# Kernel optimization log

Measured on AMD Instinct MI355X. Metric: run time of the kernel, lower is better.

The kernel has to match this reference:

```python
import jax, jax.numpy as jnp
import numpy as np

H = 64        # hidden_channels (= per-head out_channels, concat=False)
HEADS = 4
N_SRC = 50000
N_TGT = 10000
E = 250000    # edges per direction
N_LBL = 200000


def setup_inputs() -> dict:
    key = jax.random.key(0)
    ks = jax.random.split(key, 16)
    s = 1.0 / np.sqrt(H)
    # stacked TransformerConv params: leading dims [layer=2, edge_type=2]
    # edge_type 0: source->target, edge_type 1: target->source
    Wq = jax.random.normal(ks[0], (2, 2, H, HEADS * H), jnp.float32) * s
    bq = jax.random.normal(ks[1], (2, 2, HEADS * H), jnp.float32) * 0.01
    Wk = jax.random.normal(ks[2], (2, 2, H, HEADS * H), jnp.float32) * s
    bk = jax.random.normal(ks[3], (2, 2, HEADS * H), jnp.float32) * 0.01
    Wv = jax.random.normal(ks[4], (2, 2, H, HEADS * H), jnp.float32) * s
    bv = jax.random.normal(ks[5], (2, 2, HEADS * H), jnp.float32) * 0.01
    Ws = jax.random.normal(ks[6], (2, 2, H, H), jnp.float32) * s  # skip (root) lin
    bs = jax.random.normal(ks[7], (2, 2, H), jnp.float32) * 0.01
    src_emb = jax.random.normal(ks[8], (N_SRC, H), jnp.float32)
    tgt_emb = jax.random.normal(ks[9], (N_TGT, H), jnp.float32)
    node_id_source = jnp.arange(N_SRC, dtype=jnp.int32)
    node_id_target = jnp.arange(N_TGT, dtype=jnp.int32)
    edge_index_st = jnp.stack([
        jax.random.randint(ks[10], (E,), 0, N_SRC),
        jax.random.randint(ks[11], (E,), 0, N_TGT)])
    edge_index_ts = jnp.stack([
        jax.random.randint(ks[12], (E,), 0, N_TGT),
        jax.random.randint(ks[13], (E,), 0, N_SRC)])
    edge_label_index = jnp.stack([
        jax.random.randint(ks[14], (N_LBL,), 0, N_SRC),
        jax.random.randint(ks[15], (N_LBL,), 0, N_TGT)])
    return {"src_emb": src_emb, "tgt_emb": tgt_emb,
            "Wq": Wq, "bq": bq, "Wk": Wk, "bk": bk, "Wv": Wv, "bv": bv,
            "Ws": Ws, "bs": bs,
            "node_id_source": node_id_source, "node_id_target": node_id_target,
            "edge_index_st": edge_index_st, "edge_index_ts": edge_index_ts,
            "edge_label_index": edge_label_index}


def _tconv(x_src, x_dst, edge, Wq, bq, Wk, bk, Wv, bv, Ws, bs):
    """PyG TransformerConv, heads=HEADS, concat=False (mean over heads), root_weight."""
    n_dst = x_dst.shape[0]
    q = (x_dst @ Wq + bq).reshape(n_dst, HEADS, H)            # [Ndst,h,d]
    k = (x_src @ Wk + bk).reshape(x_src.shape[0], HEADS, H)   # [Nsrc,h,d]
    v = (x_src @ Wv + bv).reshape(x_src.shape[0], HEADS, H)
    src, dst = edge[0], edge[1]
    # per-edge attention scores [E,h]
    score = jnp.einsum('ehd,ehd->eh', q[dst], k[src]) / jnp.sqrt(jnp.asarray(H, x_dst.dtype))
    m = jax.ops.segment_max(score, dst, num_segments=n_dst)   # segment softmax over in-edges
    e = jnp.exp(score - m[dst])
    denom = jax.ops.segment_sum(e, dst, num_segments=n_dst)[dst]
    alpha = e / denom
    out = jax.ops.segment_sum(alpha[..., None] * v[src], dst, num_segments=n_dst)  # [Ndst,h,d]
    return out.mean(axis=1) + x_dst @ Ws + bs


def reference(src_emb, tgt_emb, Wq, bq, Wk, bk, Wv, bv, Ws, bs,
              node_id_source, node_id_target, edge_index_st, edge_index_ts,
              edge_label_index):
    xs = src_emb[node_id_source]
    xt = tgt_emb[node_id_target]
    for l in range(2):
        xt_new = _tconv(xs, xt, edge_index_st, Wq[l, 0], bq[l, 0], Wk[l, 0], bk[l, 0],
                        Wv[l, 0], bv[l, 0], Ws[l, 0], bs[l, 0])
        xs_new = _tconv(xt, xs, edge_index_ts, Wq[l, 1], bq[l, 1], Wk[l, 1], bk[l, 1],
                        Wv[l, 1], bv[l, 1], Ws[l, 1], bs[l, 1])
        if l == 0:
            xs, xt = jax.nn.relu(xs_new), jax.nn.relu(xt_new)
        else:
            xs, xt = xs_new, xt_new
    # dot-product classifier over labeled (source, target) pairs
    pred = (xs[edge_label_index[0]] * xt[edge_label_index[1]]).sum(axis=-1)  # [N_LBL]
    return pred
```

## Files before the change

### kernel.cpp

```cpp
#include <hip/hip_runtime.h>

constexpr int NSRC = 50000;
constexpr int NTGT = 10000;
constexpr int NEDGE = 250000;
constexpr int NLBL = 200000;
constexpr int HD = 64;
constexpr int NH = 4;
constexpr int QK = 256;
constexpr int NTOT = NSRC + NTGT;

typedef __attribute__((ext_vector_type(8))) short bf16x8;
typedef __attribute__((ext_vector_type(4))) float f32x4;
typedef __attribute__((ext_vector_type(2))) float f32x2;

__device__ __forceinline__ unsigned short f2bf(float f) {
  unsigned u = __float_as_uint(f);
  u += 0x7FFFu + ((u >> 16) & 1u);
  return (unsigned short)(u >> 16);
}
__device__ __forceinline__ float bf2f(unsigned short b) {
  return __uint_as_float((unsigned)b << 16);
}
struct bf4 { unsigned short x, y, z, w; };
__device__ __forceinline__ float4 bf4_to_f4(bf4 u) {
  return make_float4(bf2f(u.x), bf2f(u.y), bf2f(u.z), bf2f(u.w));
}

template<int CTRL>
__device__ __forceinline__ float dpp_addf(float x) {
  int p = __builtin_amdgcn_update_dpp(0, __float_as_int(x), CTRL, 0xf, 0xf, true);
  return x + __int_as_float(p);
}
__device__ __forceinline__ float red16(float x) {
  x = dpp_addf<0xB1>(x);
  x = dpp_addf<0x4E>(x);
  x = dpp_addf<0x141>(x);
  x = dpp_addf<0x140>(x);
  return x;
}

__device__ __forceinline__ float dot4f(float4 q, float a, float b, float c, float d) {
  return fmaf(q.w, d, fmaf(q.z, c, fmaf(q.y, b, q.x * a)));
}

__global__ __launch_bounds__(256) void setup_kernel(
    const float* __restrict__ Wq, const float* __restrict__ Wk, const float* __restrict__ Wv,
    unsigned short* __restrict__ Wtq, unsigned short* __restrict__ Wtk, unsigned short* __restrict__ Wtv,
    const float* __restrict__ semb, const int* __restrict__ sids,
    const float* __restrict__ temb, const int* __restrict__ tids,
    float* __restrict__ xs, unsigned short* __restrict__ xsb,
    float* __restrict__ xt, unsigned short* __restrict__ xtb,
    int* __restrict__ counts, int nGatherBlk) {
  __shared__ float tile[64][65];
  int b = blockIdx.x;
  int t = threadIdx.x;
  if (b < 48) {
    int mat = b >> 2, ct = b & 3;
    int grp = mat >> 2, p = mat & 3;
    const float* W = (grp == 0) ? Wq : (grp == 1) ? Wk : Wv;
    unsigned short* Wt = (grp == 0) ? Wtq : (grp == 1) ? Wtk : Wtv;
    W += (size_t)p * 16384;
    Wt += (size_t)p * 16384;
    int c = t & 63, r4 = t >> 6;
    for (int rr = 0; rr < 64; rr += 4)
      tile[rr + r4][c] = W[(size_t)(rr + r4) * 256 + ct * 64 + c];
    __syncthreads();
    for (int rr = 0; rr < 64; rr += 4) {
      int nloc = rr + r4;
      Wt[(size_t)(ct * 64 + nloc) * 64 + c] = f2bf(tile[c][nloc]);
    }
  } else if (b < 48 + nGatherBlk) {
    int i = (b - 48) * 256 + t;
    if (i < NSRC * HD) {
      float v = semb[(size_t)sids[i >> 6] * HD + (i & 63)];
      xs[i] = v;
      xsb[i] = f2bf(v);
    } else if (i < NTOT * HD) {
      int j = i - NSRC * HD;
      float v = temb[(size_t)tids[j >> 6] * HD + (j & 63)];
      xt[j] = v;
      xtb[j] = f2bf(v);
    }
  } else {
    int i = (b - 48 - nGatherBlk) * 256 + t;
    if (i < NTOT) counts[i] = 0;
  }
}


__global__ __launch_bounds__(256) void hist_all_kernel(const int* __restrict__ e_st, const int* __restrict__ e_ts,
                                                       int* __restrict__ counts) {
  int i = blockIdx.x * 256 + threadIdx.x;
  if (i < NEDGE) atomicAdd(&counts[e_st[NEDGE + i]], 1);
  else if (i < 2 * NEDGE) atomicAdd(&counts[NTGT + e_ts[NEDGE + (i - NEDGE)]], 1);
}

__global__ __launch_bounds__(256) void scan1_kernel(const int* __restrict__ counts, int* __restrict__ incl,
                                                    int* __restrict__ blocksums, int n) {
  __shared__ int wtot[4];
  int t = threadIdx.x;
  int i0 = blockIdx.x * 1024 + t * 4;
  int e0 = (i0 + 0 < n) ? counts[i0 + 0] : 0;
  int e1 = (i0 + 1 < n) ? counts[i0 + 1] : 0;
  int e2 = (i0 + 2 < n) ? counts[i0 + 2] : 0;
  int e3 = (i0 + 3 < n) ? counts[i0 + 3] : 0;
  int s0 = e0, s1 = s0 + e1, s2 = s1 + e2, s3 = s2 + e3;
  int tsum = s3;
  int inc = tsum;
#pragma unroll
  for (int o = 1; o < 64; o <<= 1) {
    int u = __shfl_up(inc, o, 64);
    if ((t & 63) >= o) inc += u;
  }
  int wave = t >> 6;
  if ((t & 63) == 63) wtot[wave] = inc;
  __syncthreads();
  int woff = 0;
#pragma unroll
  for (int w_ = 0; w_ < 4; ++w_) if (w_ < wave) woff += wtot[w_];
  int toff = woff + inc - tsum;
  if (i0 + 0 < n) incl[i0 + 0] = toff + s0;
  if (i0 + 1 < n) incl[i0 + 1] = toff + s1;
  if (i0 + 2 < n) incl[i0 + 2] = toff + s2;
  if (i0 + 3 < n) incl[i0 + 3] = toff + s3;
  if (t == 255) blocksums[blockIdx.x] = woff + inc;
}

__global__ __launch_bounds__(64) void scan2_kernel(const int* __restrict__ blocksums, int* __restrict__ boff, int nb) {
  int t = threadIdx.x;
  int v = (t < nb) ? blocksums[t] : 0;
  int inc = v;
#pragma unroll
  for (int o = 1; o < 64; o <<= 1) {
    int u = __shfl_up(inc, o, 64);
    if (t >= o) inc += u;
  }
  if (t < nb) boff[t] = inc - v;
}

__global__ __launch_bounds__(256) void scan3_kernel(const int* __restrict__ incl, const int* __restrict__ counts,
                                                    const int* __restrict__ boff, int* __restrict__ rp_st,
                                                    int* __restrict__ rp_ts, int* __restrict__ cursor) {
  int i = blockIdx.x * 256 + threadIdx.x;
  if (i < NTOT) {
    int val = incl[i] + boff[i >> 10];
    if (i < NTGT) {
      rp_st[i + 1] = val;
      cursor[i] = val - counts[i];
      if (i == 0) rp_st[0] = 0;
    } else {
      int v2 = val - NEDGE;
      rp_ts[i - NTGT + 1] = v2;
      cursor[i] = v2 - counts[i];
      if (i == NTGT) rp_ts[0] = 0;
    }
  }
}

__global__ __launch_bounds__(256) void scatter_all_kernel(const int* __restrict__ e_st, const int* __restrict__ e_ts,
                                                          int* __restrict__ cursor, int* __restrict__ es_st,
                                                          int* __restrict__ es_ts) {
  int i = blockIdx.x * 256 + threadIdx.x;
  if (i < NEDGE) {
    int d = e_st[NEDGE + i];
    int p = atomicAdd(&cursor[d], 1);
    es_st[p] = e_st[i];
  } else if (i < 2 * NEDGE) {
    int j = i - NEDGE;
    int d = e_ts[NEDGE + j];
    int p = atomicAdd(&cursor[NTGT + d], 1);
    es_ts[p] = e_ts[j];
  }
}

__global__ __launch_bounds__(256) void proj_all(
    const unsigned short* __restrict__ xsb, const unsigned short* __restrict__ xtb,
    const unsigned short* __restrict__ Wtq, const unsigned short* __restrict__ Wtk,
    const unsigned short* __restrict__ Wtv,
    const float* __restrict__ bq, const float* __restrict__ bk, const float* __restrict__ bv,
    unsigned short* __restrict__ kv_big, unsigned short* __restrict__ q_big,
    unsigned short* __restrict__ kv_small, unsigned short* __restrict__ q_small,
    int p_st, int p_ts) {
  constexpr int T = 8;
  constexpr int T1 = NSRC / 16;
  constexpr int T2 = NTGT / 16;
  constexpr int G1 = (T1 + T - 1) / T;
  constexpr int G2 = (T2 + T - 1) / T;
  int b = blockIdx.x;
  int t = threadIdx.x;
  int w = t >> 6, l = t & 63;
  int m = l & 15, qd = l >> 4;
  const unsigned short* xb; const unsigned short* WtA; const unsigned short* WtB = nullptr;
  const float* biasA; const float* biasB = nullptr;
  unsigned short* obuf;
  int tile0, ntiles, mode;
  if (b < G1) {
    xb = xsb; tile0 = b * T; ntiles = min(T, T1 - tile0); mode = 0;
    WtA = Wtk + (size_t)p_st * 16384; biasA = bk + p_st * 256;
    WtB = Wtv + (size_t)p_st * 16384; biasB = bv + p_st * 256;
    obuf = kv_big;
  } else if (b < G1 + G2) {
    xb = xtb; tile0 = (b - G1) * T; ntiles = min(T, T2 - tile0); mode = 0;
    WtA = Wtk + (size_t)p_ts * 16384; biasA = bk + p_ts * 256;
    WtB = Wtv + (size_t)p_ts * 16384; biasB = bv + p_ts * 256;
    obuf = kv_small;
  } else if (b < 2 * G1 + G2) {
    xb = xsb; tile0 = (b - G1 - G2) * T; ntiles = min(T, T1 - tile0); mode = 1;
    WtA = Wtq + (size_t)p_ts * 16384; biasA = bq + p_ts * 256;
    obuf = q_big;
  } else {
    xb = xtb; tile0 = (b - 2 * G1 - G2) * T; ntiles = min(T, T2 - tile0); mode = 1;
    WtA = Wtq + (size_t)p_st * 16384; biasA = bq + p_st * 256;
    obuf = q_small;
  }

  if (mode == 0) {
    bf16x8 wkl[4], wkh[4], wvl[4], wvh[4];
    float bkc[4], bvc[4];
#pragma unroll
    for (int i = 0; i < 4; ++i) {
      int col = (w * 4 + i) * 16 + m;
      const unsigned short* wk = WtA + (size_t)col * 64 + qd * 8;
      const unsigned short* wv = WtB + (size_t)col * 64 + qd * 8;
      wkl[i] = *(const bf16x8*)wk; wkh[i] = *(const bf16x8*)(wk + 32);
      wvl[i] = *(const bf16x8*)wv; wvh[i] = *(const bf16x8*)(wv + 32);
      bkc[i] = biasA[col]; bvc[i] = biasB[col];
    }
    const unsigned short* xr0 = xb + (size_t)(tile0 * 16 + m) * 64 + qd * 8;
    bf16x8 a_lo = *(const bf16x8*)xr0;
    bf16x8 a_hi = *(const bf16x8*)(xr0 + 32);
    for (int tt = 0; tt < ntiles; ++tt) {
      int ntt = (tt + 1 < ntiles) ? tt + 1 : tt;
      const unsigned short* xn = xb + (size_t)((tile0 + ntt) * 16 + m) * 64 + qd * 8;
      bf16x8 n_lo = *(const bf16x8*)xn;
      bf16x8 n_hi = *(const bf16x8*)(xn + 32);
      int R0 = (tile0 + tt) * 16;
#pragma unroll
      for (int i = 0; i < 4; ++i) {
        f32x4 ak = {0.f, 0.f, 0.f, 0.f}, av = {0.f, 0.f, 0.f, 0.f};
        ak = __builtin_amdgcn_mfma_f32_16x16x32_bf16(a_lo, wkl[i], ak, 0, 0, 0);
        ak = __builtin_amdgcn_mfma_f32_16x16x32_bf16(a_hi, wkh[i], ak, 0, 0, 0);
        av = __builtin_amdgcn_mfma_f32_16x16x32_bf16(a_lo, wvl[i], av, 0, 0, 0);
        av = __builtin_amdgcn_mfma_f32_16x16x32_bf16(a_hi, wvh[i], av, 0, 0, 0);
        int col = (w * 4 + i) * 16 + m;
        unsigned short* obase = obuf + (size_t)(R0 + qd * 4) * 256 + col;
#pragma unroll
        for (int r = 0; r < 4; ++r) {
          unsigned pk = __builtin_amdgcn_cvt_pk_fp8_f32(ak[r] + bkc[i], av[r] + bvc[i], 0, false);
          obase[(size_t)r * 256] = (unsigned short)pk;
        }
      }
      a_lo = n_lo; a_hi = n_hi;
    }
  } else {
    bf16x8 wql[4], wqh[4];
    float bqc[4];
#pragma unroll
    for (int i = 0; i < 4; ++i) {
      int col = (w * 4 + i) * 16 + m;
      const unsigned short* wq = WtA + (size_t)col * 64 + qd * 8;
      wql[i] = *(const bf16x8*)wq; wqh[i] = *(const bf16x8*)(wq + 32);
      bqc[i] = biasA[col];
    }
    const unsigned short* xr0 = xb + (size_t)(tile0 * 16 + m) * 64 + qd * 8;
    bf16x8 a_lo = *(const bf16x8*)xr0;
    bf16x8 a_hi = *(const bf16x8*)(xr0 + 32);
    for (int tt = 0; tt < ntiles; ++tt) {
      int ntt = (tt + 1 < ntiles) ? tt + 1 : tt;
      const unsigned short* xn = xb + (size_t)((tile0 + ntt) * 16 + m) * 64 + qd * 8;
      bf16x8 n_lo = *(const bf16x8*)xn;
      bf16x8 n_hi = *(const bf16x8*)(xn + 32);
      int R0 = (tile0 + tt) * 16;
#pragma unroll
      for (int i = 0; i < 4; ++i) {
        f32x4 acc = {0.f, 0.f, 0.f, 0.f};
        acc = __builtin_amdgcn_mfma_f32_16x16x32_bf16(a_lo, wql[i], acc, 0, 0, 0);
        acc = __builtin_amdgcn_mfma_f32_16x16x32_bf16(a_hi, wqh[i], acc, 0, 0, 0);
        int col = (w * 4 + i) * 16 + m;
        unsigned short* obase = obuf + (size_t)(R0 + qd * 4) * 256 + col;
#pragma unroll
        for (int r = 0; r < 4; ++r)
          obase[(size_t)r * 256] = f2bf(acc[r] + bqc[i]);
      }
      a_lo = n_lo; a_hi = n_hi;
    }
  }
}

__global__ __launch_bounds__(256) void skip_all(const float* __restrict__ xs, const float* __restrict__ xt,
    const float* __restrict__ Wsk, const float* __restrict__ bsk,
    float* __restrict__ xs_nxt, float* __restrict__ xt_nxt, int p_st, int p_ts, int rtS) {
  __shared__ float Xt[64][68];
  __shared__ float Wl[64][68];
  __shared__ float bias[64];
  int t = threadIdx.x;
  const float* x; const float* W; const float* bb; float* o; int N, rbase;
  if ((int)blockIdx.x < rtS) {
    x = xs; N = NSRC; rbase = blockIdx.x * 64;
    W = Wsk + (size_t)p_ts * 4096; bb = bsk + p_ts * 64; o = xs_nxt;
  } else {
    x = xt; N = NTGT; rbase = (blockIdx.x - rtS) * 64;
    W = Wsk + (size_t)p_st * 4096; bb = bsk + p_st * 64; o = xt_nxt;
  }
#pragma unroll
  for (int i = 0; i < 4; ++i) {
    int slot = i * 256 + t;
    int row = slot >> 4;
    int k4 = slot & 15;
    float4 xv = make_float4(0.f, 0.f, 0.f, 0.f);
    if (rbase + row < N) xv = *(const float4*)&x[(size_t)(rbase + row) * 64 + k4 * 4];
    Xt[k4 * 4 + 0][row] = xv.x;
    Xt[k4 * 4 + 1][row] = xv.y;
    Xt[k4 * 4 + 2][row] = xv.z;
    Xt[k4 * 4 + 3][row] = xv.w;
  }
#pragma unroll
  for (int i = 0; i < 4; ++i) {
    int slot = i * 256 + t;
    int kk = slot >> 4;
    int c4 = slot & 15;
    float4 wv = *(const float4*)&W[(size_t)kk * 64 + c4 * 4];
    *(float4*)&Wl[kk][c4 * 4] = wv;
  }
  if (t < 64) bias[t] = bb[t];
  __syncthreads();

  int c0 = (t & 15) * 4;
  int r0 = (t >> 4) * 4;
  float acc[4][4];
#pragma unroll
  for (int i = 0; i < 4; ++i)
#pragma unroll
    for (int j = 0; j < 4; ++j) acc[i][j] = 0.f;
#pragma unroll 8
  for (int kk = 0; kk < 64; ++kk) {
    float4 xv = *(const float4*)&Xt[kk][r0];
    float4 wv = *(const float4*)&Wl[kk][c0];
    float xr[4] = {xv.x, xv.y, xv.z, xv.w};
    float wc[4] = {wv.x, wv.y, wv.z, wv.w};
#pragma unroll
    for (int i = 0; i < 4; ++i)
#pragma unroll
      for (int j = 0; j < 4; ++j) acc[i][j] = fmaf(xr[i], wc[j], acc[i][j]);
  }
#pragma unroll
  for (int i = 0; i < 4; ++i) {
    int row = rbase + r0 + i;
    if (row < N) {
      float4 ov;
      ov.x = acc[i][0] + bias[c0 + 0];
      ov.y = acc[i][1] + bias[c0 + 1];
      ov.z = acc[i][2] + bias[c0 + 2];
      ov.w = acc[i][3] + bias[c0 + 3];
      *(float4*)&o[(size_t)row * 64 + c0] = ov;
    }
  }
}

__global__ __launch_bounds__(256) void agg_all(
    const unsigned short* __restrict__ q_small, const unsigned short* __restrict__ kv_big,
    const int* __restrict__ rp_st, const int* __restrict__ es_st,
    float* __restrict__ xt_nxt, unsigned short* __restrict__ xtb_nxt,
    const unsigned short* __restrict__ q_big, const unsigned short* __restrict__ kv_small,
    const int* __restrict__ rp_ts, const int* __restrict__ es_ts,
    float* __restrict__ xs_nxt, unsigned short* __restrict__ xsb_nxt,
    int relu, int stBlocks) {
  const unsigned short* q; const unsigned short* kvi; const int* rowptr; const int* eisrc;
  float* xout; unsigned short* xoutb; int node;
  int l = threadIdx.x & 63;
  int wv = __builtin_amdgcn_readfirstlane(threadIdx.x >> 6);
  if ((int)blockIdx.x < stBlocks) {
    node = blockIdx.x * 4 + wv;
    if (node >= NTGT) return;
    q = q_small; kvi = kv_big; rowptr = rp_st; eisrc = es_st; xout = xt_nxt; xoutb = xtb_nxt;
  } else {
    node = (blockIdx.x - stBlocks) * 4 + wv;
    if (node >= NSRC) return;
    q = q_big; kvi = kv_small; rowptr = rp_ts; eisrc = es_ts; xout = xs_nxt; xoutb = xsb_nxt;
  }
  int j = l & 15;
  float4 qf = bf4_to_f4(*(const bf4*)&q[(size_t)node * QK + l * 4]);
  const float QS = 0.125f * 1.44269504088896340736f;
  qf.x *= QS; qf.y *= QS; qf.z *= QS; qf.w *= QS;
  int beg = __builtin_amdgcn_readfirstlane(rowptr[node]);
  int end = __builtin_amdgcn_readfirstlane(rowptr[node + 1]);

  float lsum = 0.f;
  float4 acc = make_float4(0.f, 0.f, 0.f, 0.f);
  int p = beg;
  for (; p + 4 <= end; p += 4) {
    int s0 = __builtin_amdgcn_readfirstlane(eisrc[p]);
    int s1 = __builtin_amdgcn_readfirstlane(eisrc[p + 1]);
    int s2 = __builtin_amdgcn_readfirstlane(eisrc[p + 2]);
    int s3 = __builtin_amdgcn_readfirstlane(eisrc[p + 3]);
    uint2 a0 = ((const uint2*)(kvi + (size_t)s0 * 256))[l];
    uint2 a1 = ((const uint2*)(kvi + (size_t)s1 * 256))[l];
    uint2 a2 = ((const uint2*)(kvi + (size_t)s2 * 256))[l];
    uint2 a3 = ((const uint2*)(kvi + (size_t)s3 * 256))[l];
    f32x2 p00 = __builtin_amdgcn_cvt_pk_f32_fp8(a0.x, false);
    f32x2 p01 = __builtin_amdgcn_cvt_pk_f32_fp8(a0.x, true);
    f32x2 p02 = __builtin_amdgcn_cvt_pk_f32_fp8(a0.y, false);
    f32x2 p03 = __builtin_amdgcn_cvt_pk_f32_fp8(a0.y, true);
    f32x2 p10 = __builtin_amdgcn_cvt_pk_f32_fp8(a1.x, false);
    f32x2 p11 = __builtin_amdgcn_cvt_pk_f32_fp8(a1.x, true);
    f32x2 p12 = __builtin_amdgcn_cvt_pk_f32_fp8(a1.y, false);
    f32x2 p13 = __builtin_amdgcn_cvt_pk_f32_fp8(a1.y, true);
    f32x2 p20 = __builtin_amdgcn_cvt_pk_f32_fp8(a2.x, false);
    f32x2 p21 = __builtin_amdgcn_cvt_pk_f32_fp8(a2.x, true);
    f32x2 p22 = __builtin_amdgcn_cvt_pk_f32_fp8(a2.y, false);
    f32x2 p23 = __builtin_amdgcn_cvt_pk_f32_fp8(a2.y, true);
    f32x2 p30 = __builtin_amdgcn_cvt_pk_f32_fp8(a3.x, false);
    f32x2 p31 = __builtin_amdgcn_cvt_pk_f32_fp8(a3.x, true);
    f32x2 p32 = __builtin_amdgcn_cvt_pk_f32_fp8(a3.y, false);
    f32x2 p33 = __builtin_amdgcn_cvt_pk_f32_fp8(a3.y, true);
    float t0 = dot4f(qf, p00.x, p01.x, p02.x, p03.x);
    float t1 = dot4f(qf, p10.x, p11.x, p12.x, p13.x);
    float t2 = dot4f(qf, p20.x, p21.x, p22.x, p23.x);
    float t3 = dot4f(qf, p30.x, p31.x, p32.x, p33.x);
    t0 = red16(t0); t1 = red16(t1); t2 = red16(t2); t3 = red16(t3);
    float w0 = __builtin_amdgcn_exp2f(t0), w1 = __builtin_amdgcn_exp2f(t1);
    float w2 = __builtin_amdgcn_exp2f(t2), w3 = __builtin_amdgcn_exp2f(t3);
    lsum += (w0 + w1) + (w2 + w3);
    acc.x = fmaf(w0, p00.y, fmaf(w1, p10.y, fmaf(w2, p20.y, fmaf(w3, p30.y, acc.x))));
    acc.y = fmaf(w0, p01.y, fmaf(w1, p11.y, fmaf(w2, p21.y, fmaf(w3, p31.y, acc.y))));
    acc.z = fmaf(w0, p02.y, fmaf(w1, p12.y, fmaf(w2, p22.y, fmaf(w3, p32.y, acc.z))));
    acc.w = fmaf(w0, p03.y, fmaf(w1, p13.y, fmaf(w2, p23.y, fmaf(w3, p33.y, acc.w))));
  }
  for (; p < end; ++p) {
    int s0 = __builtin_amdgcn_readfirstlane(eisrc[p]);
    uint2 a0 = ((const uint2*)(kvi + (size_t)s0 * 256))[l];
    f32x2 p00 = __builtin_amdgcn_cvt_pk_f32_fp8(a0.x, false);
    f32x2 p01 = __builtin_amdgcn_cvt_pk_f32_fp8(a0.x, true);
    f32x2 p02 = __builtin_amdgcn_cvt_pk_f32_fp8(a0.y, false);
    f32x2 p03 = __builtin_amdgcn_cvt_pk_f32_fp8(a0.y, true);
    float s = dot4f(qf, p00.x, p01.x, p02.x, p03.x);
    s = red16(s);
    float w = __builtin_amdgcn_exp2f(s);
    lsum += w;
    acc.x = fmaf(w, p00.y, acc.x);
    acc.y = fmaf(w, p01.y, acc.y);
    acc.z = fmaf(w, p02.y, acc.z);
    acc.w = fmaf(w, p03.y, acc.w);
  }

  float inv = (lsum > 0.f) ? 1.f / lsum : 0.f;
  float4 r;
  r.x = acc.x * inv; r.y = acc.y * inv; r.z = acc.z * inv; r.w = acc.w * inv;
  r.x += __shfl_xor(r.x, 16, 64); r.x += __shfl_xor(r.x, 32, 64);
  r.y += __shfl_xor(r.y, 16, 64); r.y += __shfl_xor(r.y, 32, 64);
  r.z += __shfl_xor(r.z, 16, 64); r.z += __shfl_xor(r.z, 32, 64);
  r.w += __shfl_xor(r.w, 16, 64); r.w += __shfl_xor(r.w, 32, 64);
  if (l < 16) {
    float4 sk = *(const float4*)&xout[(size_t)node * HD + j * 4];
    float4 o;
    o.x = sk.x + 0.25f * r.x;
    o.y = sk.y + 0.25f * r.y;
    o.z = sk.z + 0.25f * r.z;
    o.w = sk.w + 0.25f * r.w;
    if (relu) {
      o.x = fmaxf(o.x, 0.f); o.y = fmaxf(o.y, 0.f);
      o.z = fmaxf(o.z, 0.f); o.w = fmaxf(o.w, 0.f);
    }
    *(float4*)&xout[(size_t)node * HD + j * 4] = o;
    bf4 ob;
    ob.x = f2bf(o.x); ob.y = f2bf(o.y); ob.z = f2bf(o.z); ob.w = f2bf(o.w);
    *(bf4*)&xoutb[(size_t)node * HD + j * 4] = ob;
  }
}

__global__ __launch_bounds__(256) void classifier_kernel(const float* __restrict__ xs, const float* __restrict__ xt,
    const int* __restrict__ ls, const int* __restrict__ lt, float* __restrict__ out, int n) {
  int g = blockIdx.x * 256 + threadIdx.x;
  int pair = g >> 4, j = g & 15;
  if (pair >= n) return;
  int a = ls[pair], b = lt[pair];
  float4 xa = *(const float4*)&xs[(size_t)a * HD + j * 4];
  float4 xb = *(const float4*)&xt[(size_t)b * HD + j * 4];
  float s = fmaf(xa.w, xb.w, fmaf(xa.z, xb.z, fmaf(xa.y, xb.y, xa.x * xb.x)));
  s = red16(s);
  if (j == 0) out[pair] = s;
}

extern "C" void kernel_launch(void* const* d_in, const int* in_sizes, int n_in,
                              void* d_out, int out_size, void* d_ws, size_t ws_size,
                              hipStream_t stream) {
  const float* src_emb = (const float*)d_in[0];
  const float* tgt_emb = (const float*)d_in[1];
  const float* Wq = (const float*)d_in[2];
  const float* bq = (const float*)d_in[3];
  const float* Wk = (const float*)d_in[4];
  const float* bk = (const float*)d_in[5];
  const float* Wv = (const float*)d_in[6];
  const float* bv = (const float*)d_in[7];
  const float* Wsk = (const float*)d_in[8];
  const float* bsk = (const float*)d_in[9];
  const int* nid_s = (const int*)d_in[10];
  const int* nid_t = (const int*)d_in[11];
  const int* e_st = (const int*)d_in[12];
  const int* e_ts = (const int*)d_in[13];
  const int* e_lbl = (const int*)d_in[14];
  float* out = (float*)d_out;

  char* ws = (char*)d_ws;
  size_t off = 0;
  auto alloc = [&](size_t bytes) -> void* {
    void* p = ws + off;
    off += (bytes + 255) & ~(size_t)255;
    return p;
  };
  unsigned short* kv_big   = (unsigned short*)alloc((size_t)NSRC * 256 * 2);
  unsigned short* q_big    = (unsigned short*)alloc((size_t)NSRC * QK * 2);
  unsigned short* kv_small = (unsigned short*)alloc((size_t)NTGT * 256 * 2);
  unsigned short* q_small  = (unsigned short*)alloc((size_t)NTGT * QK * 2);
  float* xsA = (float*)alloc((size_t)NSRC * HD * 4);
  float* xsB = (float*)alloc((size_t)NSRC * HD * 4);
  float* xtA = (float*)alloc((size_t)NTGT * HD * 4);
  float* xtB = (float*)alloc((size_t)NTGT * HD * 4);
  unsigned short* xsAb = (unsigned short*)alloc((size_t)NSRC * HD * 2);
  unsigned short* xsBb = (unsigned short*)alloc((size_t)NSRC * HD * 2);
  unsigned short* xtAb = (unsigned short*)alloc((size_t)NTGT * HD * 2);
  unsigned short* xtBb = (unsigned short*)alloc((size_t)NTGT * HD * 2);
  unsigned short* Wtq = (unsigned short*)alloc((size_t)4 * 16384 * 2);
  unsigned short* Wtk = (unsigned short*)alloc((size_t)4 * 16384 * 2);
  unsigned short* Wtv = (unsigned short*)alloc((size_t)4 * 16384 * 2);
  int* rp_st = (int*)alloc((size_t)(NTGT + 1) * 4);
  int* es_st = (int*)alloc((size_t)NEDGE * 4);
  int* rp_ts = (int*)alloc((size_t)(NSRC + 1) * 4);
  int* es_ts = (int*)alloc((size_t)NEDGE * 4);
  int* cursor = (int*)alloc((size_t)NTOT * 4);
  int* counts = (int*)alloc((size_t)NTOT * 4);
  int* incl_buf = (int*)alloc((size_t)NTOT * 4);
  int* blocksums = (int*)alloc(64 * 4);
  int* boff = (int*)alloc(64 * 4);
  (void)ws_size; (void)in_sizes; (void)n_in; (void)out_size;

  auto cdiv = [](int a, int b) { return (a + b - 1) / b; };
  const int GATHER_BLK = cdiv(NTOT * HD, 256);
  const int SETUP_BLK = 48 + GATHER_BLK + cdiv(NTOT, 256);
  const int RT_S = cdiv(NSRC, 64);
  const int RT_T = cdiv(NTGT, 64);
  const int G1 = cdiv(NSRC / 16, 8);
  const int G2 = cdiv(NTGT / 16, 8);
  const int NBLK_PROJ = 2 * (G1 + G2);
  const int ST_BLK = cdiv(NTGT, 4);
  const int NBLK_AGG = ST_BLK + cdiv(NSRC, 4);

  setup_kernel<<<SETUP_BLK, 256, 0, stream>>>(Wq, Wk, Wv, Wtq, Wtk, Wtv,
                                              src_emb, nid_s, tgt_emb, nid_t,
                                              xsA, xsAb, xtA, xtAb, counts, GATHER_BLK);

  hist_all_kernel<<<cdiv(2 * NEDGE, 256), 256, 0, stream>>>(e_st, e_ts, counts);
  scan1_kernel<<<cdiv(NTOT, 1024), 256, 0, stream>>>(counts, incl_buf, blocksums, NTOT);
  scan2_kernel<<<1, 64, 0, stream>>>(blocksums, boff, cdiv(NTOT, 1024));
  scan3_kernel<<<cdiv(NTOT, 256), 256, 0, stream>>>(incl_buf, counts, boff, rp_st, rp_ts, cursor);
  scatter_all_kernel<<<cdiv(2 * NEDGE, 256), 256, 0, stream>>>(e_st, e_ts, cursor, es_st, es_ts);

  const float* xs_cur = xsA; float* xs_nxt = xsB;
  const float* xt_cur = xtA; float* xt_nxt = xtB;
  const unsigned short* xsb_cur = xsAb; unsigned short* xsb_nxt = xsBb;
  const unsigned short* xtb_cur = xtAb; unsigned short* xtb_nxt = xtBb;
  for (int l = 0; l < 2; ++l) {
    int relu = (l == 0) ? 1 : 0;
    int p_st = l * 2 + 0, p_ts = l * 2 + 1;
    proj_all<<<NBLK_PROJ, 256, 0, stream>>>(xsb_cur, xtb_cur, Wtq, Wtk, Wtv, bq, bk, bv,
                                            kv_big, q_big, kv_small, q_small, p_st, p_ts);
    skip_all<<<RT_S + RT_T, 256, 0, stream>>>(xs_cur, xt_cur, Wsk, bsk, xs_nxt, xt_nxt, p_st, p_ts, RT_S);
    agg_all<<<NBLK_AGG, 256, 0, stream>>>(q_small, kv_big, rp_st, es_st, xt_nxt, xtb_nxt,
                                          q_big, kv_small, rp_ts, es_ts, xs_nxt, xsb_nxt,
                                          relu, ST_BLK);
    { const float* t = xs_nxt; xs_nxt = (float*)xs_cur; xs_cur = t; }
    { const float* t = xt_nxt; xt_nxt = (float*)xt_cur; xt_cur = t; }
    { const unsigned short* t = xsb_nxt; xsb_nxt = (unsigned short*)xsb_cur; xsb_cur = t; }
    { const unsigned short* t = xtb_nxt; xtb_nxt = (unsigned short*)xtb_cur; xtb_cur = t; }
  }

  classifier_kernel<<<cdiv(NLBL * 16, 256), 256, 0, stream>>>(xs_cur, xt_cur, e_lbl, e_lbl + NLBL, out, NLBL);
}
```

Baseline: 322.9 us.

## Fuse skip linear into Q projection via bf16 MFMA and drop fp32 gather

Removes the separate fp32 skip_all kernel and computes the root-weight skip projection inside proj_all's Q-projection path with bf16 MFMA, reusing the already-loaded bf16 input tile. The skip weights are transposed to bf16 in setup, and setup no longer writes fp32 copies of the gathered embeddings. This saves a kernel launch and the fp32 read of node features for each layer. The cost is bf16 precision for the skip term and extra strided fp32 stores from the Q blocks.

```diff
diff --git a/kernel.cpp b/kernel.cpp
--- a/kernel.cpp
+++ b/kernel.cpp
@@ -45,11 +45,12 @@
 
 __global__ __launch_bounds__(256) void setup_kernel(
     const float* __restrict__ Wq, const float* __restrict__ Wk, const float* __restrict__ Wv,
+    const float* __restrict__ Wsk,
     unsigned short* __restrict__ Wtq, unsigned short* __restrict__ Wtk, unsigned short* __restrict__ Wtv,
+    unsigned short* __restrict__ Wts,
     const float* __restrict__ semb, const int* __restrict__ sids,
     const float* __restrict__ temb, const int* __restrict__ tids,
-    float* __restrict__ xs, unsigned short* __restrict__ xsb,
-    float* __restrict__ xt, unsigned short* __restrict__ xtb,
+    unsigned short* __restrict__ xsb, unsigned short* __restrict__ xtb,
     int* __restrict__ counts, int nGatherBlk) {
   __shared__ float tile[64][65];
   int b = blockIdx.x;
@@ -69,20 +70,26 @@
       int nloc = rr + r4;
       Wt[(size_t)(ct * 64 + nloc) * 64 + c] = f2bf(tile[c][nloc]);
     }
-  } else if (b < 48 + nGatherBlk) {
-    int i = (b - 48) * 256 + t;
+  } else if (b < 52) {
+    int p = b - 48;
+    const float* W = Wsk + (size_t)p * 4096;
+    unsigned short* Wt = Wts + (size_t)p * 4096;
+    int c = t & 63, r4 = t >> 6;
+    for (int rr = 0; rr < 64; rr += 4)
+      tile[rr + r4][c] = W[(size_t)(rr + r4) * 64 + c];
+    __syncthreads();
+    for (int rr = 0; rr < 64; rr += 4)
+      Wt[(size_t)(rr + r4) * 64 + c] = f2bf(tile[c][rr + r4]);
+  } else if (b < 52 + nGatherBlk) {
+    int i = (b - 52) * 256 + t;
     if (i < NSRC * HD) {
-      float v = semb[(size_t)sids[i >> 6] * HD + (i & 63)];
-      xs[i] = v;
-      xsb[i] = f2bf(v);
+      xsb[i] = f2bf(semb[(size_t)sids[i >> 6] * HD + (i & 63)]);
     } else if (i < NTOT * HD) {
       int j = i - NSRC * HD;
-      float v = temb[(size_t)tids[j >> 6] * HD + (j & 63)];
-      xt[j] = v;
-      xtb[j] = f2bf(v);
+      xtb[j] = f2bf(temb[(size_t)tids[j >> 6] * HD + (j & 63)]);
     }
   } else {
-    int i = (b - 48 - nGatherBlk) * 256 + t;
+    int i = (b - 52 - nGatherBlk) * 256 + t;
     if (i < NTOT) counts[i] = 0;
   }
 }
@@ -176,10 +183,12 @@
 __global__ __launch_bounds__(256) void proj_all(
     const unsigned short* __restrict__ xsb, const unsigned short* __restrict__ xtb,
     const unsigned short* __restrict__ Wtq, const unsigned short* __restrict__ Wtk,
-    const unsigned short* __restrict__ Wtv,
+    const unsigned short* __restrict__ Wtv, const unsigned short* __restrict__ Wts,
     const float* __restrict__ bq, const float* __restrict__ bk, const float* __restrict__ bv,
+    const float* __restrict__ bsk,
     unsigned short* __restrict__ kv_big, unsigned short* __restrict__ q_big,
     unsigned short* __restrict__ kv_small, unsigned short* __restrict__ q_small,
+    float* __restrict__ xs_nxt, float* __restrict__ xt_nxt,
     int p_st, int p_ts) {
   constexpr int T = 8;
   constexpr int T1 = NSRC / 16;
@@ -193,7 +202,8 @@
   const unsigned short* xb; const unsigned short* WtA; const unsigned short* WtB = nullptr;
   const float* biasA; const float* biasB = nullptr;
   unsigned short* obuf;
-  int tile0, ntiles, mode;
+  float* skip_out = nullptr;
+  int tile0, ntiles, mode, psk = 0;
   if (b < G1) {
     xb = xsb; tile0 = b * T; ntiles = min(T, T1 - tile0); mode = 0;
     WtA = Wtk + (size_t)p_st * 16384; biasA = bk + p_st * 256;
@@ -207,11 +217,11 @@
   } else if (b < 2 * G1 + G2) {
     xb = xsb; tile0 = (b - G1 - G2) * T; ntiles = min(T, T1 - tile0); mode = 1;
     WtA = Wtq + (size_t)p_ts * 16384; biasA = bq + p_ts * 256;
-    obuf = q_big;
+    obuf = q_big; skip_out = xs_nxt; psk = p_ts;
   } else {
     xb = xtb; tile0 = (b - 2 * G1 - G2) * T; ntiles = min(T, T2 - tile0); mode = 1;
     WtA = Wtq + (size_t)p_st * 16384; biasA = bq + p_st * 256;
-    obuf = q_small;
+    obuf = q_small; skip_out = xt_nxt; psk = p_st;
   }
 
   if (mode == 0) {
@@ -262,6 +272,11 @@
       wql[i] = *(const bf16x8*)wq; wqh[i] = *(const bf16x8*)(wq + 32);
       bqc[i] = biasA[col];
     }
+    int scol = w * 16 + m;
+    const unsigned short* ws = Wts + (size_t)psk * 4096 + (size_t)scol * 64 + qd * 8;
+    bf16x8 wsl_ = *(const bf16x8*)ws;
+    bf16x8 wsh_ = *(const bf16x8*)(ws + 32);
+    float bsc = bsk[psk * 64 + scol];
     const unsigned short* xr0 = xb + (size_t)(tile0 * 16 + m) * 64 + qd * 8;
     bf16x8 a_lo = *(const bf16x8*)xr0;
     bf16x8 a_hi = *(const bf16x8*)(xr0 + 32);
@@ -282,77 +297,16 @@
         for (int r = 0; r < 4; ++r)
           obase[(size_t)r * 256] = f2bf(acc[r] + bqc[i]);
       }
+      {
+        f32x4 sa = {0.f, 0.f, 0.f, 0.f};
+        sa = __builtin_amdgcn_mfma_f32_16x16x32_bf16(a_lo, wsl_, sa, 0, 0, 0);
+        sa = __builtin_amdgcn_mfma_f32_16x16x32_bf16(a_hi, wsh_, sa, 0, 0, 0);
+        float* so = skip_out + (size_t)(R0 + qd * 4) * 64 + scol;
+#pragma unroll
+        for (int r = 0; r < 4; ++r)
+          so[(size_t)r * 64] = sa[r] + bsc;
+      }
       a_lo = n_lo; a_hi = n_hi;
-    }
-  }
-}
-
-__global__ __launch_bounds__(256) void skip_all(const float* __restrict__ xs, const float* __restrict__ xt,
-    const float* __restrict__ Wsk, const float* __restrict__ bsk,
-    float* __restrict__ xs_nxt, float* __restrict__ xt_nxt, int p_st, int p_ts, int rtS) {
-  __shared__ float Xt[64][68];
-  __shared__ float Wl[64][68];
-  __shared__ float bias[64];
-  int t = threadIdx.x;
-  const float* x; const float* W; const float* bb; float* o; int N, rbase;
-  if ((int)blockIdx.x < rtS) {
-    x = xs; N = NSRC; rbase = blockIdx.x * 64;
-    W = Wsk + (size_t)p_ts * 4096; bb = bsk + p_ts * 64; o = xs_nxt;
-  } else {
-    x = xt; N = NTGT; rbase = (blockIdx.x - rtS) * 64;
-    W = Wsk + (size_t)p_st * 4096; bb = bsk + p_st * 64; o = xt_nxt;
-  }
-#pragma unroll
-  for (int i = 0; i < 4; ++i) {
-    int slot = i * 256 + t;
-    int row = slot >> 4;
-    int k4 = slot & 15;
-    float4 xv = make_float4(0.f, 0.f, 0.f, 0.f);
-    if (rbase + row < N) xv = *(const float4*)&x[(size_t)(rbase + row) * 64 + k4 * 4];
-    Xt[k4 * 4 + 0][row] = xv.x;
-    Xt[k4 * 4 + 1][row] = xv.y;
-    Xt[k4 * 4 + 2][row] = xv.z;
-    Xt[k4 * 4 + 3][row] = xv.w;
-  }
-#pragma unroll
-  for (int i = 0; i < 4; ++i) {
-    int slot = i * 256 + t;
-    int kk = slot >> 4;
-    int c4 = slot & 15;
-    float4 wv = *(const float4*)&W[(size_t)kk * 64 + c4 * 4];
-    *(float4*)&Wl[kk][c4 * 4] = wv;
-  }
-  if (t < 64) bias[t] = bb[t];
-  __syncthreads();
-
-  int c0 = (t & 15) * 4;
-  int r0 = (t >> 4) * 4;
-  float acc[4][4];
-#pragma unroll
-  for (int i = 0; i < 4; ++i)
-#pragma unroll
-    for (int j = 0; j < 4; ++j) acc[i][j] = 0.f;
-#pragma unroll 8
-  for (int kk = 0; kk < 64; ++kk) {
-    float4 xv = *(const float4*)&Xt[kk][r0];
-    float4 wv = *(const float4*)&Wl[kk][c0];
-    float xr[4] = {xv.x, xv.y, xv.z, xv.w};
-    float wc[4] = {wv.x, wv.y, wv.z, wv.w};
-#pragma unroll
-    for (int i = 0; i < 4; ++i)
-#pragma unroll
-      for (int j = 0; j < 4; ++j) acc[i][j] = fmaf(xr[i], wc[j], acc[i][j]);
-  }
-#pragma unroll
-  for (int i = 0; i < 4; ++i) {
-    int row = rbase + r0 + i;
-    if (row < N) {
-      float4 ov;
-      ov.x = acc[i][0] + bias[c0 + 0];
-      ov.y = acc[i][1] + bias[c0 + 1];
-      ov.z = acc[i][2] + bias[c0 + 2];
-      ov.w = acc[i][3] + bias[c0 + 3];
-      *(float4*)&o[(size_t)row * 64 + c0] = ov;
     }
   }
 }
@@ -523,6 +477,7 @@
   unsigned short* Wtq = (unsigned short*)alloc((size_t)4 * 16384 * 2);
   unsigned short* Wtk = (unsigned short*)alloc((size_t)4 * 16384 * 2);
   unsigned short* Wtv = (unsigned short*)alloc((size_t)4 * 16384 * 2);
+  unsigned short* Wts = (unsigned short*)alloc((size_t)4 * 4096 * 2);
   int* rp_st = (int*)alloc((size_t)(NTGT + 1) * 4);
   int* es_st = (int*)alloc((size_t)NEDGE * 4);
   int* rp_ts = (int*)alloc((size_t)(NSRC + 1) * 4);
@@ -536,18 +491,16 @@
 
   auto cdiv = [](int a, int b) { return (a + b - 1) / b; };
   const int GATHER_BLK = cdiv(NTOT * HD, 256);
-  const int SETUP_BLK = 48 + GATHER_BLK + cdiv(NTOT, 256);
-  const int RT_S = cdiv(NSRC, 64);
-  const int RT_T = cdiv(NTGT, 64);
+  const int SETUP_BLK = 52 + GATHER_BLK + cdiv(NTOT, 256);
   const int G1 = cdiv(NSRC / 16, 8);
   const int G2 = cdiv(NTGT / 16, 8);
   const int NBLK_PROJ = 2 * (G1 + G2);
   const int ST_BLK = cdiv(NTGT, 4);
   const int NBLK_AGG = ST_BLK + cdiv(NSRC, 4);
 
-  setup_kernel<<<SETUP_BLK, 256, 0, stream>>>(Wq, Wk, Wv, Wtq, Wtk, Wtv,
+  setup_kernel<<<SETUP_BLK, 256, 0, stream>>>(Wq, Wk, Wv, Wsk, Wtq, Wtk, Wtv, Wts,
                                               src_emb, nid_s, tgt_emb, nid_t,
-                                              xsA, xsAb, xtA, xtAb, counts, GATHER_BLK);
+                                              xsAb, xtAb, counts, GATHER_BLK);
 
   hist_all_kernel<<<cdiv(2 * NEDGE, 256), 256, 0, stream>>>(e_st, e_ts, counts);
   scan1_kernel<<<cdiv(NTOT, 1024), 256, 0, stream>>>(counts, incl_buf, blocksums, NTOT);
@@ -555,21 +508,22 @@
   scan3_kernel<<<cdiv(NTOT, 256), 256, 0, stream>>>(incl_buf, counts, boff, rp_st, rp_ts, cursor);
   scatter_all_kernel<<<cdiv(2 * NEDGE, 256), 256, 0, stream>>>(e_st, e_ts, cursor, es_st, es_ts);
 
-  const float* xs_cur = xsA; float* xs_nxt = xsB;
-  const float* xt_cur = xtA; float* xt_nxt = xtB;
+  float* xs_cur = xsA; float* xs_nxt = xsB;
+  float* xt_cur = xtA; float* xt_nxt = xtB;
   const unsigned short* xsb_cur = xsAb; unsigned short* xsb_nxt = xsBb;
   const unsigned short* xtb_cur = xtAb; unsigned short* xtb_nxt = xtBb;
   for (int l = 0; l < 2; ++l) {
     int relu = (l == 0) ? 1 : 0;
     int p_st = l * 2 + 0, p_ts = l * 2 + 1;
-    proj_all<<<NBLK_PROJ, 256, 0, stream>>>(xsb_cur, xtb_cur, Wtq, Wtk, Wtv, bq, bk, bv,
-                                            kv_big, q_big, kv_small, q_small, p_st, p_ts);
-    skip_all<<<RT_S + RT_T, 256, 0, stream>>>(xs_cur, xt_cur, Wsk, bsk, xs_nxt, xt_nxt, p_st, p_ts, RT_S);
+    proj_all<<<NBLK_PROJ, 256, 0, stream>>>(xsb_cur, xtb_cur, Wtq, Wtk, Wtv, Wts,
+                                            bq, bk, bv, bsk,
+                                            kv_big, q_big, kv_small, q_small,
+                                            xs_nxt, xt_nxt, p_st, p_ts);
     agg_all<<<NBLK_AGG, 256, 0, stream>>>(q_small, kv_big, rp_st, es_st, xt_nxt, xtb_nxt,
                                           q_big, kv_small, rp_ts, es_ts, xs_nxt, xsb_nxt,
                                           relu, ST_BLK);
-    { const float* t = xs_nxt; xs_nxt = (float*)xs_cur; xs_cur = t; }
-    { const float* t = xt_nxt; xt_nxt = (float*)xt_cur; xt_cur = t; }
+    { float* t = xs_nxt; xs_nxt = xs_cur; xs_cur = t; }
+    { float* t = xt_nxt; xt_nxt = xt_cur; xt_cur = t; }
     { const unsigned short* t = xsb_nxt; xsb_nxt = (unsigned short*)xsb_cur; xsb_cur = t; }
     { const unsigned short* t = xtb_nxt; xtb_nxt = (unsigned short*)xtb_cur; xtb_cur = t; }
   }
```

Result: faster. 298.2 us (-7.6%).
